# Performance work log

Hardware: AMD Instinct MI355X
Metric: run time of the kernel (lower is better)

The kernel has to match this reference:

```python
import jax, jax.numpy as jnp
import numpy as np

B, S, D = 8, 4096, 1024
H, DH = 16, 64
DM = H * DH  # d_model = 1024


def setup_inputs() -> dict:
    key = jax.random.key(0)
    k0, k1, k2, k3 = jax.random.split(key, 4)
    x = jax.random.uniform(k0, (B, S, D), dtype=jnp.float32)
    # nn.Linear weights (stored here pre-transposed as [in, out]).
    Wq = jax.random.normal(k1, (D, DM), dtype=jnp.float32) * 0.02
    Wkv = jax.random.normal(k2, (D, 2 * DM), dtype=jnp.float32) * 0.02
    Wlin = jax.random.normal(k3, (DM, DM), dtype=jnp.float32) * 0.02
    blin = jnp.zeros((DM,), dtype=jnp.float32)
    return {"x": x, "Wq": Wq, "Wkv": Wkv, "Wlin": Wlin, "blin": blin}


def reference(x, Wq, Wkv, Wlin, blin):
    scale = DH ** (-0.5)
    # projections; cond_dim=None => cond = x (self attention), mask=None
    q = (x @ Wq).reshape(B, S, H, DH)          # [B,S,H,DH]
    kv = (x @ Wkv).reshape(B, S, H, 2 * DH)    # [B,S,H,2*DH]
    k, v = kv[..., :DH], kv[..., DH:]
    # dual softmax: q over feature dim (scaled), k over sequence dim
    q = jax.nn.softmax(q, axis=-1) * scale
    k = jax.nn.softmax(k, axis=1)              # seq axis in BSHD layout
    # context = k^T @ v per (batch, head): [B,H,DH,DH]
    context = jnp.einsum('bshd,bshe->bhde', k, v)
    # out = q @ context: [B,S,H,DH]
    out = jnp.einsum('bshd,bhde->bshe', q, context).reshape(B, S, DM)
    return out @ Wlin + blin
```

## Files before the change

### kernel.cpp

```cpp
#include <hip/hip_runtime.h>
#include <hip/hip_bf16.h>
#include <cstdint>

using bf16 = __hip_bfloat16;
typedef __attribute__((ext_vector_type(8))) short bf16x8;
typedef __attribute__((ext_vector_type(4))) float f32x4;

struct alignas(16) B8 { bf16 h[8]; };
struct alignas(8)  B4 { bf16 h[4]; };

__device__ __forceinline__ void gll16(const void* g, void* l) {
  __builtin_amdgcn_global_load_lds((__attribute__((address_space(1))) void*)g,
                                   (__attribute__((address_space(3))) void*)l,
                                   16, 0, 0);
}

__global__ void cast_f32_bf16(const float* __restrict__ in, bf16* __restrict__ out, long long n) {
  long long i = ((long long)blockIdx.x * blockDim.x + threadIdx.x) * 8;
  if (i >= n) return;
  float4 v0 = *(const float4*)(in + i);
  float4 v1 = *(const float4*)(in + i + 4);
  B8 o;
  o.h[0] = __float2bfloat16(v0.x); o.h[1] = __float2bfloat16(v0.y);
  o.h[2] = __float2bfloat16(v0.z); o.h[3] = __float2bfloat16(v0.w);
  o.h[4] = __float2bfloat16(v1.x); o.h[5] = __float2bfloat16(v1.y);
  o.h[6] = __float2bfloat16(v1.z); o.h[7] = __float2bfloat16(v1.w);
  *(B8*)(out + i) = o;
}

__global__ void tcast(const float* __restrict__ W, bf16* __restrict__ WT, int K, int N) {
  __shared__ float tile[32][33];
  int k0 = blockIdx.y * 32, n0 = blockIdx.x * 32;
  int tx = threadIdx.x, ty = threadIdx.y;
  for (int yy = ty; yy < 32; yy += 8)
    tile[yy][tx] = W[(size_t)(k0 + yy) * N + n0 + tx];
  __syncthreads();
  for (int yy = ty; yy < 32; yy += 8)
    WT[(size_t)(n0 + yy) * K + k0 + tx] = __float2bfloat16(tile[tx][yy]);
}

__device__ __forceinline__ void gemm_mainloop_256(
    const bf16* __restrict__ aop0, const bf16* __restrict__ aop1,
    const bf16* __restrict__ bop0, const bf16* __restrict__ bop1,
    bf16* ldsA, bf16* ldsB, int wd0, int wd1,
    int arow, int brow, int fc, f32x4 (&acc)[8][4])
{
#define STAGE_A(slot, ko) do { gll16(aop0 + (ko), ldsA + (slot) * 8192 + wd0); \
                               gll16(aop1 + (ko), ldsA + (slot) * 8192 + wd1); } while (0)
#define STAGE_B(slot, ko) do { gll16(bop0 + (ko), ldsB + (slot) * 8192 + wd0); \
                               gll16(bop1 + (ko), ldsB + (slot) * 8192 + wd1); } while (0)
#define AFRAG(slot, i) (*(const bf16x8*)(ldsA + (slot) * 8192 + (arow + (i) * 16) * 32 + fc))
#define BFRAG(slot, j) (*(const bf16x8*)(ldsB + (slot) * 8192 + (brow + (j) * 16) * 32 + fc))

  STAGE_A(0, 0); STAGE_B(0, 0);
  STAGE_A(1, 32); STAGE_B(1, 32);
  asm volatile("s_waitcnt vmcnt(4)" ::: "memory");
  __builtin_amdgcn_s_barrier();
  __builtin_amdgcn_sched_barrier(0);

  #pragma unroll 2
  for (int kt = 0; kt < 16; ++kt) {
    const int s0 = (2 * kt) & 3, s1 = (2 * kt + 1) & 3;
    const int p0 = (2 * kt + 2) & 3, p1 = (2 * kt + 3) & 3;
    const int ko = (kt + 1) * 64;
    const bool more = kt < 15;
    bf16x8 a[4], b[4];

    #pragma unroll
    for (int j = 0; j < 4; j++) b[j] = BFRAG(s0, j);
    #pragma unroll
    for (int i = 0; i < 4; i++) a[i] = AFRAG(s0, i);
    if (more) STAGE_A(p0, ko);
    __builtin_amdgcn_s_barrier();
    asm volatile("s_waitcnt lgkmcnt(0)" ::: "memory");
    __builtin_amdgcn_sched_barrier(0);
    __builtin_amdgcn_s_setprio(1);
    #pragma unroll
    for (int i = 0; i < 4; i++)
      #pragma unroll
      for (int j = 0; j < 4; j++)
        acc[i][j] = __builtin_amdgcn_mfma_f32_16x16x32_bf16(a[i], b[j], acc[i][j], 0, 0, 0);
    __builtin_amdgcn_s_setprio(0);
    __builtin_amdgcn_s_barrier();

    #pragma unroll
    for (int i = 0; i < 4; i++) a[i] = AFRAG(s0, i + 4);
    if (more) STAGE_B(p0, ko);
    __builtin_amdgcn_s_barrier();
    asm volatile("s_waitcnt lgkmcnt(0)" ::: "memory");
    __builtin_amdgcn_sched_barrier(0);
    __builtin_amdgcn_s_setprio(1);
    #pragma unroll
    for (int i = 0; i < 4; i++)
      #pragma unroll
      for (int j = 0; j < 4; j++)
        acc[i + 4][j] = __builtin_amdgcn_mfma_f32_16x16x32_bf16(a[i], b[j], acc[i + 4][j], 0, 0, 0);
    __builtin_amdgcn_s_setprio(0);
    if (more) { asm volatile("s_waitcnt vmcnt(4)" ::: "memory"); }
    else      { asm volatile("s_waitcnt vmcnt(0)" ::: "memory"); }
    __builtin_amdgcn_s_barrier();
    __builtin_amdgcn_sched_barrier(0);

    #pragma unroll
    for (int j = 0; j < 4; j++) b[j] = BFRAG(s1, j);
    #pragma unroll
    for (int i = 0; i < 4; i++) a[i] = AFRAG(s1, i);
    if (more) STAGE_A(p1, ko + 32);
    __builtin_amdgcn_s_barrier();
    asm volatile("s_waitcnt lgkmcnt(0)" ::: "memory");
    __builtin_amdgcn_sched_barrier(0);
    __builtin_amdgcn_s_setprio(1);
    #pragma unroll
    for (int i = 0; i < 4; i++)
      #pragma unroll
      for (int j = 0; j < 4; j++)
        acc[i][j] = __builtin_amdgcn_mfma_f32_16x16x32_bf16(a[i], b[j], acc[i][j], 0, 0, 0);
    __builtin_amdgcn_s_setprio(0);
    __builtin_amdgcn_s_barrier();

    #pragma unroll
    for (int i = 0; i < 4; i++) a[i] = AFRAG(s1, i + 4);
    if (more) STAGE_B(p1, ko + 32);
    __builtin_amdgcn_s_barrier();
    asm volatile("s_waitcnt lgkmcnt(0)" ::: "memory");
    __builtin_amdgcn_sched_barrier(0);
    __builtin_amdgcn_s_setprio(1);
    #pragma unroll
    for (int i = 0; i < 4; i++)
      #pragma unroll
      for (int j = 0; j < 4; j++)
        acc[i + 4][j] = __builtin_amdgcn_mfma_f32_16x16x32_bf16(a[i], b[j], acc[i + 4][j], 0, 0, 0);
    __builtin_amdgcn_s_setprio(0);
    if (more) { asm volatile("s_waitcnt vmcnt(4)" ::: "memory"); }
    else      { asm volatile("s_waitcnt vmcnt(0)" ::: "memory"); }
    __builtin_amdgcn_s_barrier();
    __builtin_amdgcn_sched_barrier(0);
  }
#undef STAGE_A
#undef STAGE_B
#undef AFRAG
#undef BFRAG
}

constexpr int QKV_NT = 12;

__global__ __launch_bounds__(512, 2)
void gemm_qkv(const bf16* __restrict__ A, const bf16* __restrict__ BT,
              bf16* __restrict__ Yq, float* __restrict__ ctxAcc)
{
  __shared__ __align__(16) union {
    struct { bf16 a[4 * 8192]; bf16 b[4 * 8192]; } g;
    struct { bf16 ekT[2][16384]; bf16 vT[2][16384]; } c;
  } sm;

  const int t = threadIdx.x;
  const int wave = t >> 6, lane = t & 63;
  const int lr = lane & 15, kq = lane >> 4;
  const int wm = wave >> 2, wn = wave & 3;
  const int bid = (int)blockIdx.x;
  const int swz = (bid & 7) * 192 + (bid >> 3);
  const int bm = swz / QKV_NT, bn = swz % QKV_NT;
  const int m0 = bm * 256, n0 = bn * 256;

  const int srow = t >> 2;
  const int cl = (t & 3) ^ ((srow ^ (srow >> 2)) & 3);
  const bf16* aop0 = A + (size_t)(m0 + srow) * 1024 + cl * 8;
  const bf16* aop1 = A + (size_t)(m0 + 128 + srow) * 1024 + cl * 8;
  const bf16* bop0 = BT + (size_t)(n0 + srow) * 1024 + cl * 8;
  const bf16* bop1 = BT + (size_t)(n0 + 128 + srow) * 1024 + cl * 8;
  const int wd0 = wave * 512;
  const int wd1 = 4096 + wave * 512;

  const int fc = (kq ^ ((lr ^ (lr >> 2)) & 3)) * 8;
  const int arow = wm * 128 + lr;
  const int brow = wn * 64 + lr;

  const f32x4 zero = {0.f, 0.f, 0.f, 0.f};
  f32x4 acc[8][4];
  #pragma unroll
  for (int i = 0; i < 8; i++)
    #pragma unroll
    for (int j = 0; j < 4; j++) acc[i][j] = zero;

  gemm_mainloop_256(aop0, aop1, bop0, bop1, sm.g.a, sm.g.b, wd0, wd1,
                    arow, brow, fc, acc);

  if (bn < 4) {
    #pragma unroll
    for (int i = 0; i < 8; i++) {
      #pragma unroll
      for (int r = 0; r < 4; r++) {
        float m = fmaxf(fmaxf(acc[i][0][r], acc[i][1][r]),
                        fmaxf(acc[i][2][r], acc[i][3][r]));
        m = fmaxf(m, __shfl_xor(m, 1));
        m = fmaxf(m, __shfl_xor(m, 2));
        m = fmaxf(m, __shfl_xor(m, 4));
        m = fmaxf(m, __shfl_xor(m, 8));
        float ex[4]; float s = 0.f;
        #pragma unroll
        for (int j = 0; j < 4; j++) { ex[j] = __expf(acc[i][j][r] - m); s += ex[j]; }
        s += __shfl_xor(s, 1);
        s += __shfl_xor(s, 2);
        s += __shfl_xor(s, 4);
        s += __shfl_xor(s, 8);
        const float inv = 0.125f / s;
        const int row = m0 + wm * 128 + i * 16 + kq * 4 + r;
        bf16* yrow = Yq + (size_t)row * 1024 + n0 + wn * 64;
        #pragma unroll
        for (int j = 0; j < 4; j++)
          yrow[j * 16 + lr] = __float2bfloat16(ex[j] * inv);
      }
    }
  } else {
    const int bb = m0 >> 12;
    const int h0 = (n0 - 1024) >> 7;
    const int hloc = wn >> 1, isV = wn & 1;
    bf16* const dstT = (isV ? sm.c.vT[hloc] : sm.c.ekT[hloc]);

    float zp[4] = {0.f, 0.f, 0.f, 0.f};
    #pragma unroll
    for (int i = 0; i < 8; i++) {
      const int sbase = wm * 128 + i * 16 + kq * 4;
      const int sxo = sbase >> 3;
      const int sby = (sbase & 7) * 2;
      #pragma unroll
      for (int j = 0; j < 4; j++) {
        const int d = j * 16 + lr;
        B4 pk;
        if (!isV) {
          #pragma unroll
          for (int r = 0; r < 4; r++) {
            float e = __expf(acc[i][j][r]);
            zp[j] += e;
            pk.h[r] = __float2bfloat16(e);
          }
        } else {
          #pragma unroll
          for (int r = 0; r < 4; r++) pk.h[r] = __float2bfloat16(acc[i][j][r]);
        }
        *(B4*)((char*)dstT + d * 512 + ((sxo ^ (d & 7)) << 4) + sby) = pk;
      }
    }

    if (!isV) {
      #pragma unroll
      for (int j = 0; j < 4; j++) {
        zp[j] += __shfl_xor(zp[j], 16);
        zp[j] += __shfl_xor(zp[j], 32);
      }
      if (kq == 0) {
        float* zb = ctxAcc + (size_t)(bb * 16 + h0 + hloc) * 4160 + 4096;
        #pragma unroll
        for (int j = 0; j < 4; j++) atomicAdd(zb + j * 16 + lr, zp[j]);
      }
    }
    __syncthreads();

    const int hh = wave >> 2, dq = wave & 3;
    const bf16* const ek = sm.c.ekT[hh];
    const bf16* const vv = sm.c.vT[hh];
    f32x4 racc[4] = {zero, zero, zero, zero};
    #pragma unroll
    for (int ks = 0; ks < 8; ks++) {
      const int ch = ks * 4 + kq;
      bf16x8 af = *(const bf16x8*)((const char*)ek + (dq * 16 + lr) * 512 + ((ch ^ (lr & 7)) << 4));
      #pragma unroll
      for (int j = 0; j < 4; j++) {
        bf16x8 bfr = *(const bf16x8*)((const char*)vv + (j * 16 + lr) * 512 + ((ch ^ (lr & 7)) << 4));
        racc[j] = __builtin_amdgcn_mfma_f32_16x16x32_bf16(af, bfr, racc[j], 0, 0, 0);
      }
    }
    float* cb = ctxAcc + (size_t)(bb * 16 + h0 + hh) * 4160;
    #pragma unroll
    for (int j = 0; j < 4; j++) {
      #pragma unroll
      for (int r = 0; r < 4; r++)
        atomicAdd(cb + (dq * 16 + kq * 4 + r) * 64 + j * 16 + lr, racc[j][r]);
    }
  }
}

__global__ __launch_bounds__(256) void make_w2t(const float* __restrict__ ctxAcc,
                                                const bf16* __restrict__ WlinT,
                                                bf16* __restrict__ W2T) {
  const int nc = blockIdx.x;
  const int bh = blockIdx.y;
  const int b = bh >> 4, h = bh & 15;
  const int t = threadIdx.x, lane = t & 63, w = t >> 6;
  const float* src = ctxAcc + (size_t)bh * 4160;
  const float invz = 1.0f / src[4096 + lane];
  float creg[64];
  const float* crow = src + lane * 64;
  #pragma unroll
  for (int e4 = 0; e4 < 16; e4++) {
    float4 v = *(const float4*)(crow + e4 * 4);
    creg[e4 * 4 + 0] = v.x * invz; creg[e4 * 4 + 1] = v.y * invz;
    creg[e4 * 4 + 2] = v.z * invz; creg[e4 * 4 + 3] = v.w * invz;
  }
  for (int i = 0; i < 16; i++) {
    const int n = nc * 64 + w * 16 + i;
    const bf16* wrow = WlinT + (size_t)n * 1024 + h * 64;
    float acc = 0.f;
    #pragma unroll
    for (int e8 = 0; e8 < 8; e8++) {
      B8 v = *(const B8*)(wrow + e8 * 8);
      #pragma unroll
      for (int j = 0; j < 8; j++) acc += creg[e8 * 8 + j] * __bfloat162float(v.h[j]);
    }
    W2T[((size_t)b * 1024 + n) * 1024 + h * 64 + lane] = __float2bfloat16(acc);
  }
}

__global__ __launch_bounds__(512, 2)
void gemm_out(const bf16* __restrict__ Aall, const bf16* __restrict__ BTall,
              float* __restrict__ Call, const float* __restrict__ bias)
{
  __shared__ __align__(16) struct { bf16 a[4 * 8192]; bf16 b[4 * 8192]; } sm;
  const int t = threadIdx.x;
  const int wave = t >> 6, lane = t & 63;
  const int lr = lane & 15, kq = lane >> 4;
  const int wm = wave >> 2, wn = wave & 3;
  const int bid = (int)blockIdx.x;
  const int swz = (bid & 7) * 64 + (bid >> 3);
  const int bz = swz >> 6;
  const int r  = swz & 63;
  const int bm = r >> 2, bn = r & 3;
  const int m0 = bm * 256, n0 = bn * 256;
  const bf16* A  = Aall  + (size_t)bz * 4096 * 1024;
  const bf16* BT = BTall + (size_t)bz * 1024 * 1024;
  float* C       = Call  + (size_t)bz * 4096 * 1024;

  const int srow = t >> 2;
  const int cl = (t & 3) ^ ((srow ^ (srow >> 2)) & 3);
  const bf16* aop0 = A + (size_t)(m0 + srow) * 1024 + cl * 8;
  const bf16* aop1 = A + (size_t)(m0 + 128 + srow) * 1024 + cl * 8;
  const bf16* bop0 = BT + (size_t)(n0 + srow) * 1024 + cl * 8;
  const bf16* bop1 = BT + (size_t)(n0 + 128 + srow) * 1024 + cl * 8;
  const int wd0 = wave * 512;
  const int wd1 = 4096 + wave * 512;

  const int fc = (kq ^ ((lr ^ (lr >> 2)) & 3)) * 8;
  const int arow = wm * 128 + lr;
  const int brow = wn * 64 + lr;

  const f32x4 zero = {0.f, 0.f, 0.f, 0.f};
  f32x4 acc[8][4];
  #pragma unroll
  for (int i = 0; i < 8; i++)
    #pragma unroll
    for (int j = 0; j < 4; j++) acc[i][j] = zero;

  gemm_mainloop_256(aop0, aop1, bop0, bop1, sm.a, sm.b, wd0, wd1,
                    arow, brow, fc, acc);

  float bv[4];
  #pragma unroll
  for (int j = 0; j < 4; j++) bv[j] = bias[n0 + wn * 64 + j * 16 + lr];
  #pragma unroll
  for (int i = 0; i < 8; i++) {
    const int row0 = m0 + wm * 128 + i * 16 + kq * 4;
    #pragma unroll
    for (int j = 0; j < 4; j++) {
      const int col = n0 + wn * 64 + j * 16 + lr;
      #pragma unroll
      for (int r2 = 0; r2 < 4; r2++)
        C[(size_t)(row0 + r2) * 1024 + col] = acc[i][j][r2] + bv[j];
    }
  }
}

extern "C" void kernel_launch(void* const* d_in, const int* in_sizes, int n_in,
                              void* d_out, int out_size, void* d_ws, size_t ws_size,
                              hipStream_t stream) {
  (void)in_sizes; (void)n_in; (void)out_size; (void)ws_size;
  const float* x    = (const float*)d_in[0];
  const float* Wq   = (const float*)d_in[1];
  const float* Wkv  = (const float*)d_in[2];
  const float* Wlin = (const float*)d_in[3];
  const float* blin = (const float*)d_in[4];
  float* out = (float*)d_out;

  bf16* x_bf  = (bf16*)d_ws;
  bf16* WTc   = x_bf + 33554432;
  bf16* WlinT = WTc + 3145728;
  bf16* Yq    = WlinT + 1048576;
  bf16* W2T   = Yq + 33554432;
  float* ctxAcc = (float*)(W2T + 8388608);

  cast_f32_bf16<<<16384, 256, 0, stream>>>(x, x_bf, 33554432LL);
  tcast<<<dim3(32, 32), dim3(32, 8), 0, stream>>>(Wq, WTc, 1024, 1024);
  tcast<<<dim3(64, 32), dim3(32, 8), 0, stream>>>(Wkv, WTc + 1048576, 1024, 2048);
  tcast<<<dim3(32, 32), dim3(32, 8), 0, stream>>>(Wlin, WlinT, 1024, 1024);

  hipMemsetAsync(ctxAcc, 0, (size_t)128 * 4160 * sizeof(float), stream);

  gemm_qkv<<<dim3(128 * QKV_NT), 512, 0, stream>>>(x_bf, WTc, Yq, ctxAcc);
  make_w2t<<<dim3(16, 128), 256, 0, stream>>>(ctxAcc, WlinT, W2T);
  gemm_out<<<dim3(512), 512, 0, stream>>>(Yq, W2T, out, blin);
}
```

Measured before the change: 403.4 us.

## Restructure GEMM mainloop to one barrier per K-step with interleaved fragment loads

The bf16 GEMM main loop is rewritten so each 32-wide K half-step has a single vmcnt wait and workgroup barrier, where it previously had four. The wait sits at the top of the step, and the prefetch of the next A tile into the ring slot two ahead is issued right after it. The second group of A fragments is now read from LDS between MFMA rows, overlapping LDS reads with matrix math. This is meant to cut barrier stalls and idle MFMA time in the shared main loop. The cost is heavier reliance on the 4-slot ring spacing for correctness, plus a trailing __syncthreads; the bias value is also hoisted into a local in the epilogue.

```diff
diff --git a/kernel.cpp b/kernel.cpp
--- a/kernel.cpp
+++ b/kernel.cpp
@@ -54,88 +54,55 @@
 
   STAGE_A(0, 0); STAGE_B(0, 0);
   STAGE_A(1, 32); STAGE_B(1, 32);
-  asm volatile("s_waitcnt vmcnt(4)" ::: "memory");
-  __builtin_amdgcn_s_barrier();
-  __builtin_amdgcn_sched_barrier(0);
 
   #pragma unroll 2
   for (int kt = 0; kt < 16; ++kt) {
-    const int s0 = (2 * kt) & 3, s1 = (2 * kt + 1) & 3;
-    const int p0 = (2 * kt + 2) & 3, p1 = (2 * kt + 3) & 3;
-    const int ko = (kt + 1) * 64;
     const bool more = kt < 15;
-    bf16x8 a[4], b[4];
-
-    #pragma unroll
-    for (int j = 0; j < 4; j++) b[j] = BFRAG(s0, j);
-    #pragma unroll
-    for (int i = 0; i < 4; i++) a[i] = AFRAG(s0, i);
-    if (more) STAGE_A(p0, ko);
-    __builtin_amdgcn_s_barrier();
-    asm volatile("s_waitcnt lgkmcnt(0)" ::: "memory");
-    __builtin_amdgcn_sched_barrier(0);
-    __builtin_amdgcn_s_setprio(1);
-    #pragma unroll
-    for (int i = 0; i < 4; i++)
-      #pragma unroll
-      for (int j = 0; j < 4; j++)
-        acc[i][j] = __builtin_amdgcn_mfma_f32_16x16x32_bf16(a[i], b[j], acc[i][j], 0, 0, 0);
-    __builtin_amdgcn_s_setprio(0);
-    __builtin_amdgcn_s_barrier();
-
-    #pragma unroll
-    for (int i = 0; i < 4; i++) a[i] = AFRAG(s0, i + 4);
-    if (more) STAGE_B(p0, ko);
-    __builtin_amdgcn_s_barrier();
-    asm volatile("s_waitcnt lgkmcnt(0)" ::: "memory");
-    __builtin_amdgcn_sched_barrier(0);
-    __builtin_amdgcn_s_setprio(1);
-    #pragma unroll
-    for (int i = 0; i < 4; i++)
-      #pragma unroll
-      for (int j = 0; j < 4; j++)
-        acc[i + 4][j] = __builtin_amdgcn_mfma_f32_16x16x32_bf16(a[i], b[j], acc[i + 4][j], 0, 0, 0);
-    __builtin_amdgcn_s_setprio(0);
-    if (more) { asm volatile("s_waitcnt vmcnt(4)" ::: "memory"); }
-    else      { asm volatile("s_waitcnt vmcnt(0)" ::: "memory"); }
-    __builtin_amdgcn_s_barrier();
-    __builtin_amdgcn_sched_barrier(0);
-
-    #pragma unroll
-    for (int j = 0; j < 4; j++) b[j] = BFRAG(s1, j);
-    #pragma unroll
-    for (int i = 0; i < 4; i++) a[i] = AFRAG(s1, i);
-    if (more) STAGE_A(p1, ko + 32);
-    __builtin_amdgcn_s_barrier();
-    asm volatile("s_waitcnt lgkmcnt(0)" ::: "memory");
-    __builtin_amdgcn_sched_barrier(0);
-    __builtin_amdgcn_s_setprio(1);
-    #pragma unroll
-    for (int i = 0; i < 4; i++)
-      #pragma unroll
-      for (int j = 0; j < 4; j++)
-        acc[i][j] = __builtin_amdgcn_mfma_f32_16x16x32_bf16(a[i], b[j], acc[i][j], 0, 0, 0);
-    __builtin_amdgcn_s_setprio(0);
-    __builtin_amdgcn_s_barrier();
-
-    #pragma unroll
-    for (int i = 0; i < 4; i++) a[i] = AFRAG(s1, i + 4);
-    if (more) STAGE_B(p1, ko + 32);
-    __builtin_amdgcn_s_barrier();
-    asm volatile("s_waitcnt lgkmcnt(0)" ::: "memory");
-    __builtin_amdgcn_sched_barrier(0);
-    __builtin_amdgcn_s_setprio(1);
-    #pragma unroll
-    for (int i = 0; i < 4; i++)
-      #pragma unroll
-      for (int j = 0; j < 4; j++)
-        acc[i + 4][j] = __builtin_amdgcn_mfma_f32_16x16x32_bf16(a[i], b[j], acc[i + 4][j], 0, 0, 0);
-    __builtin_amdgcn_s_setprio(0);
-    if (more) { asm volatile("s_waitcnt vmcnt(4)" ::: "memory"); }
-    else      { asm volatile("s_waitcnt vmcnt(0)" ::: "memory"); }
-    __builtin_amdgcn_s_barrier();
-    __builtin_amdgcn_sched_barrier(0);
-  }
+    #pragma unroll
+    for (int h = 0; h < 2; ++h) {
+      const int sh = (2 * kt + h) & 3;
+      const int ph = (2 * kt + 2 + h) & 3;
+      const int ko = (kt + 1) * 64 + h * 32;
+
+      if (more || h == 0) { asm volatile("s_waitcnt vmcnt(4)" ::: "memory"); }
+      else               { asm volatile("s_waitcnt vmcnt(0)" ::: "memory"); }
+      __builtin_amdgcn_s_barrier();
+      __builtin_amdgcn_sched_barrier(0);
+
+      if (more) STAGE_A(ph, ko);
+
+      bf16x8 a[4], b[4];
+      #pragma unroll
+      for (int j = 0; j < 4; j++) b[j] = BFRAG(sh, j);
+      #pragma unroll
+      for (int i = 0; i < 4; i++) a[i] = AFRAG(sh, i);
+      asm volatile("s_waitcnt lgkmcnt(0)" ::: "memory");
+      __builtin_amdgcn_sched_barrier(0);
+
+      __builtin_amdgcn_s_setprio(1);
+      #pragma unroll
+      for (int i = 0; i < 4; i++) {
+        #pragma unroll
+        for (int j = 0; j < 4; j++)
+          acc[i][j] = __builtin_amdgcn_mfma_f32_16x16x32_bf16(a[i], b[j], acc[i][j], 0, 0, 0);
+        a[i] = AFRAG(sh, i + 4);
+      }
+      __builtin_amdgcn_s_setprio(0);
+
+      if (more) STAGE_B(ph, ko);
+      asm volatile("s_waitcnt lgkmcnt(0)" ::: "memory");
+      __builtin_amdgcn_sched_barrier(0);
+
+      __builtin_amdgcn_s_setprio(1);
+      #pragma unroll
+      for (int i = 0; i < 4; i++)
+        #pragma unroll
+        for (int j = 0; j < 4; j++)
+          acc[i + 4][j] = __builtin_amdgcn_mfma_f32_16x16x32_bf16(a[i], b[j], acc[i + 4][j], 0, 0, 0);
+      __builtin_amdgcn_s_setprio(0);
+    }
+  }
+  __syncthreads();
 #undef STAGE_A
 #undef STAGE_B
 #undef AFRAG
@@ -362,9 +329,10 @@
     #pragma unroll
     for (int j = 0; j < 4; j++) {
       const int col = n0 + wn * 64 + j * 16 + lr;
+      const float bvj = bv[j];
       #pragma unroll
       for (int r2 = 0; r2 < 4; r2++)
-        C[(size_t)(row0 + r2) * 1024 + col] = acc[i][j][r2] + bv[j];
+        C[(size_t)(row0 + r2) * 1024 + col] = acc[i][j][r2] + bvj;
     }
   }
 }
```

New measurement: 390.8 us. 3.1% less time.
